# Kernel optimization log

Measured on AMD Instinct MI355X. Metric: run time of the kernel, lower is better.

Reference implementation:

```python
import jax, jax.numpy as jnp
import numpy as np

ODE_UNFOLDS = 6  # ncps LTCCell default
EPS = 1e-8


def setup_inputs() -> dict:
    key = jax.random.key(0)
    ks = jax.random.split(key, 24)
    B, C, H, W = 8192, 3, 23, 30   # 8*(H-1)*(W-1) = 5104 matches fc1
    S, N, M = 32, 19, 1            # sensory size, NCP units, motor outputs
    u = lambda k, shape, lo, hi: jax.random.uniform(k, shape, jnp.float32, lo, hi)
    # NCP wiring: binary sparsity masks (|adjacency|) and +/-1 reversal polarities
    sensory_mask = (jax.random.uniform(ks[20], (S, N)) < 0.6).astype(jnp.float32)
    mask = (jax.random.uniform(ks[21], (N, N)) < 0.5).astype(jnp.float32)
    sensory_erev = sensory_mask * jnp.sign(jax.random.normal(ks[22], (S, N)))
    erev = mask * jnp.sign(jax.random.normal(ks[23], (N, N)))
    return {
        "x": jax.random.normal(ks[0], (B, C, H, W), jnp.float32),
        "conv_w": jax.random.normal(ks[1], (8, C, 2, 2), jnp.float32) * 0.1,
        "conv_b": jnp.zeros((8,), jnp.float32),
        "fc1_w": jax.random.normal(ks[2], (64, 5104), jnp.float32) * 0.02,
        "fc1_b": jnp.zeros((64,), jnp.float32),
        "fc2_w": jax.random.normal(ks[3], (32, 64), jnp.float32) * 0.1,
        "fc2_b": jnp.zeros((32,), jnp.float32),
        "input_w": jnp.ones((S,), jnp.float32),
        "input_b": jnp.zeros((S,), jnp.float32),
        "sensory_w": u(ks[4], (S, N), 0.001, 1.0),
        "sensory_mu": u(ks[5], (S, N), 0.3, 0.8),
        "sensory_sigma": u(ks[6], (S, N), 3.0, 8.0),
        "sensory_erev": sensory_erev,
        "sensory_mask": sensory_mask,
        "w": u(ks[7], (N, N), 0.001, 1.0),
        "mu": u(ks[8], (N, N), 0.3, 0.8),
        "sigma": u(ks[9], (N, N), 3.0, 8.0),
        "erev": erev,
        "mask": mask,
        "gleak": u(ks[10], (N,), 0.001, 1.0),
        "vleak": u(ks[11], (N,), -0.2, 0.2),
        "cm": u(ks[12], (N,), 0.4, 0.6),
        "output_w": jnp.ones((M,), jnp.float32),
        "output_b": jnp.zeros((M,), jnp.float32),
    }


def _forward(x, conv_w, conv_b, fc1_w, fc1_b, fc2_w, fc2_b,
             input_w, input_b,
             sensory_w, sensory_mu, sensory_sigma, sensory_erev, sensory_mask,
             w, mu, sigma, erev, mask,
             gleak, vleak, cm, output_w, output_b):
    # conv + ELU
    y = jax.lax.conv_general_dilated(
        x, conv_w, window_strides=(1, 1), padding="VALID",
        dimension_numbers=("NCHW", "OIHW", "NCHW"))
    y = jax.nn.elu(y + conv_b[None, :, None, None])
    y = y.reshape(y.shape[0], -1)                 # (B, 5104)
    y = jax.nn.relu(y @ fc1_w.T + fc1_b)          # (B, 64); dropout = identity (eval)
    y = y @ fc2_w.T + fc2_b                       # (B, 32)

    # LTC: 2D input -> unbatched sequence of length B (ncps semantics)
    seq = y * input_w + input_b                   # affine input mapping, (T, S)
    # sensory synapse effects depend only on inputs -> precompute vectorized
    s_act = (jax.nn.softplus(sensory_w)
             * jax.nn.sigmoid(sensory_sigma * (seq[:, :, None] - sensory_mu))
             * sensory_mask)                      # (T, S, N)
    wnum_s = jnp.sum(s_act * sensory_erev, axis=1)  # (T, N)
    wden_s = jnp.sum(s_act, axis=1)                 # (T, N)

    cm_t = jax.nn.softplus(cm) * ODE_UNFOLDS      # cm / (elapsed_time=1 / unfolds)
    w_param = jax.nn.softplus(w) * mask           # (N, N), mask folded in
    g = jax.nn.softplus(gleak)

    def step(v, ins):
        wn_s, wd_s = ins
        for _ in range(ODE_UNFOLDS):              # implicit-Euler fused unfolds
            gate = jax.nn.sigmoid(sigma * (v[:, None] - mu))  # (src N, tgt N)
            w_act = w_param * gate
            wn = jnp.sum(w_act * erev, axis=0) + wn_s
            wd = jnp.sum(w_act, axis=0) + wd_s
            v = (cm_t * v + g * vleak + wn) / (cm_t + g + wd + EPS)
        return v, v

    v0 = jnp.zeros((w.shape[0],), seq.dtype)
    _, states = jax.lax.scan(step, v0, (wnum_s, wden_s))  # (T, N)
    # motor readout: first motor_size neurons + affine output mapping
    out = states[:, :output_w.shape[0]] * output_w + output_b  # (T, 1)
    return out


def reference(x, conv_w, conv_b, fc1_w, fc1_b, fc2_w, fc2_b,
              input_w, input_b,
              sensory_w, sensory_mu, sensory_sigma, sensory_erev, sensory_mask,
              w, mu, sigma, erev, mask,
              gleak, vleak, cm, output_w, output_b):
    return _forward(x, conv_w, conv_b, fc1_w, fc1_b, fc2_w, fc2_b,
                    input_w, input_b,
                    sensory_w, sensory_mu, sensory_sigma, sensory_erev, sensory_mask,
                    w, mu, sigma, erev, mask,
                    gleak, vleak, cm, output_w, output_b)
```

## Files before the change

kernel.cpp:

```cpp
#include <hip/hip_runtime.h>
#include <hip/hip_bf16.h>
#include <math.h>

#define L2E 1.4426950408889634f
#define T_STEPS 8192
#define KTOT 5104
#define EPS_LTC 1e-8f
#define KP 5120

#define SCAN_CHUNKS 1024
#define S_PER  8
#define WARM   16

#define WS_BASE_FLOATS 315584
#define WS_NEED_BSP    2573056

typedef __attribute__((ext_vector_type(8))) short bfrag;
typedef __attribute__((ext_vector_type(4))) float ffrag;
typedef __attribute__((ext_vector_type(4))) float fvec4;

__device__ __forceinline__ float softplus_f(float x) {
    return log1pf(expf(-fabsf(x))) + fmaxf(x, 0.f);
}

__device__ __forceinline__ unsigned short bf_hi(float f) {
    unsigned u = __float_as_uint(f);
    u = u + 0x7FFFu + ((u >> 16) & 1u);
    return (unsigned short)(u >> 16);
}

__device__ __forceinline__ float elu_f(float x) {
    return (x > 0.f) ? x : (__builtin_amdgcn_exp2f(x * L2E) - 1.f);
}

__device__ __forceinline__ float half_sum(float x) {
#if __has_builtin(__builtin_amdgcn_permlane32_swap)
    auto r = __builtin_amdgcn_permlane32_swap(__float_as_int(x), __float_as_int(x),
                                              false, false);
    return __int_as_float(r[0]) + __int_as_float(r[1]);
#else
    int pidx = ((threadIdx.x & 63) ^ 32) * 4;
    return x + __int_as_float(
        __builtin_amdgcn_ds_bpermute(pidx, __float_as_int(x)));
#endif
}

__global__ __launch_bounds__(640) void k0_combined(
    const float* __restrict__ sw, const float* __restrict__ smu,
    const float* __restrict__ ssig, const float* __restrict__ serev,
    const float* __restrict__ smask,
    const float* __restrict__ w, const float* __restrict__ mu,
    const float* __restrict__ sigma, const float* __restrict__ erev,
    const float* __restrict__ mask,
    const float* __restrict__ gleak, const float* __restrict__ vleak,
    const float* __restrict__ cm,
    float* __restrict__ sc1, float* __restrict__ sc0,
    float* __restrict__ swe, float* __restrict__ swp,
    float* __restrict__ rc1, float* __restrict__ rc0,
    float* __restrict__ rwe, float* __restrict__ rwp,
    float* __restrict__ neu,
    const float* __restrict__ fc1_w,
    unsigned short* __restrict__ bhi, unsigned short* __restrict__ blo,
    int use_bsp)
{
    if (blockIdx.x == 512) {
        int t = threadIdx.x;
        if (t < 608) {
            float sp = softplus_f(sw[t]);
            float c1 = ssig[t] * L2E;
            sc1[t] = c1;
            sc0[t] = c1 * smu[t];
            swe[t] = sp * serev[t];
            swp[t] = sp * smask[t];
        }
        if (t < 361) {
            float wp = softplus_f(w[t]) * mask[t];
            float c1 = sigma[t] * L2E;
            rc1[t] = c1;
            rc0[t] = c1 * mu[t];
            rwe[t] = wp * erev[t];
            rwp[t] = wp;
        }
        if (t < 64) {
            if (t < 19) {
                float g   = softplus_f(gleak[t]);
                float cmt = softplus_f(cm[t]) * 6.f;
                neu[t]       = cmt;
                neu[64 + t]  = g * vleak[t];
                neu[128 + t] = cmt + g + EPS_LTC;
            } else {
                neu[t] = 0.f; neu[64 + t] = 0.f; neu[128 + t] = 1.f;
            }
        }
        return;
    }
    if (!use_bsp) return;
    int i = blockIdx.x * 640 + threadIdx.x;
    int n, o, r;
    float v;
    if (i < 326656) {
        n = i / 5104;
        int k = i - n * 5104;
        o = k / 638;
        r = k - o * 638;
        v = fc1_w[i];
    } else {
        int p = i - 326656;
        n = p >> 4;
        int rem = p & 15;
        o = rem >> 1;
        r = 638 + (rem & 1);
        v = 0.f;
    }
    int kc = r >> 2, q = o >> 1;
    int j  = (o & 1) * 4 + (r & 3);
    int g  = (((kc * 16 + q * 4 + (n >> 4)) * 16) + (n & 15)) * 8 + j;
    unsigned short h = bf_hi(v);
    bhi[g] = h;
    blo[g] = bf_hi(v - __uint_as_float((unsigned)h << 16));
}

#define LOADWIN(KC, WB) do {                                                  \
    int r0_  = (KC) * 4;                                                      \
    int oh0_ = (r0_ * 565) >> 14;                                             \
    int ow0_ = r0_ - oh0_ * 29;                                               \
    _Pragma("unroll")                                                         \
    for (int cc_ = 0; cc_ < 3; cc_++) {                                       \
        const float* a0_ = xls + cc_ * 690 + oh0_ * 30 + ow0_;                \
        fvec4 v0_, v1_;                                                       \
        __builtin_memcpy(&v0_, a0_, 16);                                      \
        __builtin_memcpy(&v1_, a0_ + 30, 16);                                 \
        WB[cc_*10+0]=v0_.x; WB[cc_*10+1]=v0_.y; WB[cc_*10+2]=v0_.z;           \
        WB[cc_*10+3]=v0_.w; WB[cc_*10+4]=a0_[4];                              \
        WB[cc_*10+5]=v1_.x; WB[cc_*10+6]=v1_.y; WB[cc_*10+7]=v1_.z;           \
        WB[cc_*10+8]=v1_.w; WB[cc_*10+9]=a0_[34];                             \
    }                                                                         \
} while (0)

#define PACKA(Y0, Y1, AH, AL) do {                                            \
    _Pragma("unroll")                                                         \
    for (int j_ = 0; j_ < 4; j_++) {                                          \
        unsigned short h0_ = bf_hi(Y0[j_]);                                   \
        AH[j_] = (short)h0_;                                                  \
        AL[j_] = (short)bf_hi(Y0[j_] - __uint_as_float((unsigned)h0_ << 16)); \
        unsigned short h1_ = bf_hi(Y1[j_]);                                   \
        AH[4+j_] = (short)h1_;                                                \
        AL[4+j_] = (short)bf_hi(Y1[j_] - __uint_as_float((unsigned)h1_ << 16));\
    }                                                                         \
} while (0)

#define BUILDA_FAST(WB, AH, AL) do {                                          \
    float y0_[4], y1_[4];                                                     \
    _Pragma("unroll")                                                         \
    for (int rr_ = 0; rr_ < 4; rr_++) {                                       \
        float a0v_ = cb0, a1v_ = cb1;                                         \
        _Pragma("unroll")                                                     \
        for (int cc_ = 0; cc_ < 3; cc_++) {                                   \
            float x00_ = WB[cc_*10+rr_],   x01_ = WB[cc_*10+rr_+1];           \
            float x10_ = WB[cc_*10+5+rr_], x11_ = WB[cc_*10+6+rr_];           \
            a0v_ = fmaf(x00_, cw0[cc_*4+0], a0v_);                            \
            a0v_ = fmaf(x01_, cw0[cc_*4+1], a0v_);                            \
            a0v_ = fmaf(x10_, cw0[cc_*4+2], a0v_);                            \
            a0v_ = fmaf(x11_, cw0[cc_*4+3], a0v_);                            \
            a1v_ = fmaf(x00_, cw1[cc_*4+0], a1v_);                            \
            a1v_ = fmaf(x01_, cw1[cc_*4+1], a1v_);                            \
            a1v_ = fmaf(x10_, cw1[cc_*4+2], a1v_);                            \
            a1v_ = fmaf(x11_, cw1[cc_*4+3], a1v_);                            \
        }                                                                     \
        y0_[rr_] = elu_f(a0v_);                                               \
        y1_[rr_] = elu_f(a1v_);                                               \
    }                                                                         \
    PACKA(y0_, y1_, AH, AL);                                                  \
} while (0)

#define BUILDA_SLOW(KC, AH, AL) do {                                          \
    float y0_[4], y1_[4];                                                     \
    int r0_ = (KC) * 4;                                                       \
    _Pragma("unroll")                                                         \
    for (int rr_ = 0; rr_ < 4; rr_++) {                                       \
        int r_ = r0_ + rr_;                                                   \
        if (r_ < 638) {                                                       \
            int oh_ = (r_ * 565) >> 14;                                       \
            const float* xp_ = xls + oh_ * 30 + (r_ - oh_ * 29);              \
            float a0v_ = cb0, a1v_ = cb1;                                     \
            _Pragma("unroll")                                                 \
            for (int cc_ = 0; cc_ < 3; cc_++) {                               \
                float x00_ = xp_[cc_*690],    x01_ = xp_[cc_*690+1];          \
                float x10_ = xp_[cc_*690+30], x11_ = xp_[cc_*690+31];         \
                a0v_ = fmaf(x00_, cw0[cc_*4+0], a0v_);                        \
                a0v_ = fmaf(x01_, cw0[cc_*4+1], a0v_);                        \
                a0v_ = fmaf(x10_, cw0[cc_*4+2], a0v_);                        \
                a0v_ = fmaf(x11_, cw0[cc_*4+3], a0v_);                        \
                a1v_ = fmaf(x00_, cw1[cc_*4+0], a1v_);                        \
                a1v_ = fmaf(x01_, cw1[cc_*4+1], a1v_);                        \
                a1v_ = fmaf(x10_, cw1[cc_*4+2], a1v_);                        \
                a1v_ = fmaf(x11_, cw1[cc_*4+3], a1v_);                        \
            }                                                                 \
            y0_[rr_] = elu_f(a0v_);                                           \
            y1_[rr_] = elu_f(a1v_);                                           \
        } else { y0_[rr_] = 0.f; y1_[rr_] = 0.f; }                            \
    }                                                                         \
    PACKA(y0_, y1_, AH, AL);                                                  \
} while (0)

#define LOADB(KC, BH, BL) do {                                                \
    _Pragma("unroll")                                                         \
    for (int nt_ = 0; nt_ < 4; nt_++) {                                       \
        size_t off_ = ((size_t)((KC) * 16 + q * 4 + nt_) * 16 + mn) * 8;      \
        BH[nt_] = *(const bfrag*)(bhi + off_);                                \
        BL[nt_] = *(const bfrag*)(blo + off_);                                \
    }                                                                         \
} while (0)

#define MFMA3(AH, AL, BH, BL) do {                                            \
    _Pragma("unroll")                                                         \
    for (int nt_ = 0; nt_ < 4; nt_++) {                                       \
        acc[nt_] = __builtin_amdgcn_mfma_f32_16x16x32_bf16(AH, BH[nt_], acc[nt_], 0, 0, 0); \
        acc[nt_] = __builtin_amdgcn_mfma_f32_16x16x32_bf16(AH, BL[nt_], acc[nt_], 0, 0, 0); \
        acc[nt_] = __builtin_amdgcn_mfma_f32_16x16x32_bf16(AL, BH[nt_], acc[nt_], 0, 0, 0); \
    }                                                                         \
} while (0)

__global__ __launch_bounds__(512, 1) void k12_frontend(
    const float* __restrict__ x, const float* __restrict__ conv_w,
    const float* __restrict__ conv_b,
    const float* __restrict__ fc1_w, const float* __restrict__ fc1_b,
    const float* __restrict__ fc2_w, const float* __restrict__ fc2_b,
    const float* __restrict__ iw, const float* __restrict__ ib,
    const float* __restrict__ sc1, const float* __restrict__ sc0,
    const float* __restrict__ swe, const float* __restrict__ swp,
    const unsigned short* __restrict__ bhi,
    const unsigned short* __restrict__ blo, int use_bsp,
    float* __restrict__ wn_s, float* __restrict__ wd_s)
{
    __shared__ __align__(16) float smem[33120];
    float* redS = smem;
    float* hS   = smem + 8192;
    float* w2S  = smem + 9312;
    float* seqS = smem + 11392;

    const int t    = threadIdx.x;
    const int b0   = blockIdx.x * 16;
    const int lane = t & 63;
    const int wv   = t >> 6;
    const int q    = lane >> 4;
    const int mn   = lane & 15;
    const int o0   = 2 * q;

    {
        const float* xg = x + (size_t)b0 * 2070;
        #pragma unroll
        for (int i = 0; i < 16; i++) {
            int idx = i * 512 + t;
            fvec4 v;
            __builtin_memcpy(&v, xg + (size_t)idx * 4, 16);
            __builtin_memcpy(smem + (size_t)idx * 4, &v, 16);
        }
        if (t < 88) {
            int idx = 8192 + t;
            fvec4 v;
            __builtin_memcpy(&v, xg + (size_t)idx * 4, 16);
            __builtin_memcpy(smem + (size_t)idx * 4, &v, 16);
        }
    }
    __syncthreads();

    float cw0[12], cw1[12];
    #pragma unroll
    for (int i = 0; i < 12; i++) {
        cw0[i] = conv_w[o0 * 12 + i];
        cw1[i] = conv_w[o0 * 12 + 12 + i];
    }
    const float cb0 = conv_b[o0], cb1 = conv_b[o0 + 1];
    const float* xls = smem + mn * 2070;

    ffrag acc[4];
    #pragma unroll
    for (int nt = 0; nt < 4; nt++) acc[nt] = (ffrag){0.f, 0.f, 0.f, 0.f};

    const int kc0 = wv * 20;

    auto isFast = [](int kc) {
        int r0 = kc * 4;
        int oh0 = (r0 * 565) >> 14;
        int ow0 = r0 - oh0 * 29;
        return (ow0 <= 25 && r0 + 3 <= 637);
    };

    if (use_bsp) {
        float winA[30], winB[30];
        bfrag bh0[4], bl0[4], bh1[4], bl1[4];
        bool fA = isFast(kc0);
        if (fA) LOADWIN(kc0, winA);
        LOADB(kc0, bh0, bl0);
        for (int kk = 0; kk < 20; kk += 2) {
            const int kc = kc0 + kk;
            bool fB = isFast(kc + 1);
            LOADB(kc + 1, bh1, bl1);
            if (fB) LOADWIN(kc + 1, winB);
            {
                bfrag a_hi, a_lo;
                if (fA) { BUILDA_FAST(winA, a_hi, a_lo); }
                else    { BUILDA_SLOW(kc, a_hi, a_lo); }
                MFMA3(a_hi, a_lo, bh0, bl0);
            }
            fA = isFast(kc + 2);
            if (kk + 2 < 20) {
                LOADB(kc + 2, bh0, bl0);
                if (fA) LOADWIN(kc + 2, winA);
            }
            {
                bfrag a_hi, a_lo;
                if (fB) { BUILDA_FAST(winB, a_hi, a_lo); }
                else    { BUILDA_SLOW(kc + 1, a_hi, a_lo); }
                MFMA3(a_hi, a_lo, bh1, bl1);
            }
        }
    } else {
        for (int kk = 0; kk < 20; kk++) {
            const int kc = kc0 + kk;
            bfrag a_hi, a_lo;
            BUILDA_SLOW(kc, a_hi, a_lo);
            #pragma unroll
            for (int nt = 0; nt < 4; nt++) {
                int n = nt * 16 + mn;
                bfrag b_h, b_l;
                #pragma unroll
                for (int j = 0; j < 8; j++) {
                    int o = o0 + (j >> 2);
                    int r = kc * 4 + (j & 3);
                    float vv = (r < 638) ? fc1_w[(size_t)n * KTOT + o * 638 + r] : 0.f;
                    unsigned short h = bf_hi(vv);
                    b_h[j] = (short)h;
                    b_l[j] = (short)bf_hi(vv - __uint_as_float((unsigned)h << 16));
                }
                acc[nt] = __builtin_amdgcn_mfma_f32_16x16x32_bf16(a_hi, b_h, acc[nt], 0, 0, 0);
                acc[nt] = __builtin_amdgcn_mfma_f32_16x16x32_bf16(a_hi, b_l, acc[nt], 0, 0, 0);
                acc[nt] = __builtin_amdgcn_mfma_f32_16x16x32_bf16(a_lo, b_h, acc[nt], 0, 0, 0);
            }
        }
    }

    __syncthreads();

    #pragma unroll
    for (int nt = 0; nt < 4; nt++) {
        int n = nt * 16 + mn;
        #pragma unroll
        for (int rg = 0; rg < 4; rg++) {
            int m = q * 4 + rg;
            redS[(wv * 16 + m) * 64 + n] = acc[nt][rg];
        }
    }
    __syncthreads();
    #pragma unroll
    for (int e = 0; e < 2; e++) {
        int flat = e * 512 + t;
        int m = flat >> 6, n = flat & 63;
        float s = 0.f;
        #pragma unroll
        for (int p = 0; p < 8; p++) s += redS[(p * 16 + m) * 64 + n];
        hS[m * 68 + n] = fmaxf(s + fc1_b[n], 0.f);
    }
    #pragma unroll
    for (int e = 0; e < 4; e++) {
        int flat = e * 512 + t;
        int s = flat >> 6, n = flat & 63;
        w2S[s * 65 + n] = fc2_w[flat];
    }
    __syncthreads();

    {
        int s = t & 31, bl = t >> 5;
        float a2 = fc2_b[s];
        #pragma unroll 8
        for (int n = 0; n < 64; n++)
            a2 = fmaf(hS[bl * 68 + n], w2S[s * 65 + n], a2);
        seqS[bl * 33 + s] = a2 * iw[s] + ib[s];
    }
    __syncthreads();

    if (t < 304) {
        int n = t % 19, bl = t / 19;
        float wn = 0.f, wd = 0.f;
        #pragma unroll
        for (int s = 0; s < 32; s++) {
            float xx = sc0[s * 19 + n] - sc1[s * 19 + n] * seqS[bl * 33 + s];
            float ee = __builtin_amdgcn_exp2f(xx);
            float uu = __builtin_amdgcn_rcpf(1.f + ee);
            wn = fmaf(swe[s * 19 + n], uu, wn);
            wd = fmaf(swp[s * 19 + n], uu, wd);
        }
        wn_s[(b0 + bl) * 19 + n] = wn;
        wd_s[(b0 + bl) * 19 + n] = wd;
    }
}

__global__ __launch_bounds__(64, 1) void k3p2_scan(
    const float* __restrict__ wn_s, const float* __restrict__ wd_s,
    const float* __restrict__ rc1, const float* __restrict__ rc0,
    const float* __restrict__ rwe, const float* __restrict__ rwp,
    const float* __restrict__ neu,
    const float* __restrict__ out_w, const float* __restrict__ out_b,
    float* __restrict__ out)
{
    const int l    = threadIdx.x;
    const int col  = l & 31;
    const int p    = l >> 5;
    const int cidx = (col < 19) ? col : 0;
    const bool hi  = (l >= 32);

    float ca[10], cb[10], cwe[10], cwp[10];
    #pragma unroll
    for (int j = 0; j < 10; j++) {
        int s = p * 10 + j;
        bool e = (col < 19) && (s < 19);
        int idx = e ? (s * 19 + col) : 0;
        ca[j]  = e ? rc1[idx] : 0.f;
        cb[j]  = e ? rc0[idx] : 0.f;
        cwe[j] = e ? rwe[idx] : 0.f;
        cwp[j] = e ? rwp[idx] : 0.f;
    }

    const float cmt  = neu[cidx];
    const float gvl  = neu[64 + cidx];
    const float den0 = neu[128 + cidx];
    const float owv  = out_w[0];
    const float obv  = out_b[0];

    const int c       = blockIdx.x;
    const int s_out   = c * S_PER;
    const int s_begin = (s_out > WARM) ? (s_out - WARM) : 0;
    const int s_end   = s_out + S_PER;

    float v = 0.f;
    float wnc = wn_s[s_begin * 19 + cidx];
    float wdc = wd_s[s_begin * 19 + cidx];

    for (int tt = s_begin; tt < s_end; tt++) {
        int nt = (tt + 1 < T_STEPS) ? (tt + 1) : (T_STEPS - 1);
        float wnn = wn_s[nt * 19 + cidx];
        float wdn = wd_s[nt * 19 + cidx];

        #pragma unroll
        for (int u = 0; u < 6; u++) {
            float vs[10];
            #pragma unroll
            for (int j = 0; j < 10; j++) {
                float v0 = __int_as_float(
                    __builtin_amdgcn_readlane(__float_as_int(v), j));
                float v1 = __int_as_float(
                    __builtin_amdgcn_readlane(__float_as_int(v), 10 + j));
                vs[j] = hi ? v1 : v0;
            }

            float tn[10], td[10];
            #pragma unroll
            for (int j = 0; j < 10; j++) {
                float xx = fmaf(-ca[j], vs[j], cb[j]);
                float ee = __builtin_amdgcn_exp2f(xx);
                float uu = __builtin_amdgcn_rcpf(1.f + ee);
                tn[j] = cwe[j] * uu;
                td[j] = cwp[j] * uu;
            }
            float pn = (((tn[0] + tn[1]) + (tn[2] + tn[3]))
                      + ((tn[4] + tn[5]) + (tn[6] + tn[7])))
                      + (tn[8] + tn[9]);
            float pd = (((td[0] + td[1]) + (td[2] + td[3]))
                      + ((td[4] + td[5]) + (td[6] + td[7])))
                      + (td[8] + td[9]);

            pn = half_sum(pn);
            pd = half_sum(pd);

            float num = fmaf(cmt, v, gvl) + (pn + wnc);
            float den = den0 + pd + wdc;
            v = num * __builtin_amdgcn_rcpf(den);
        }
        if (l == 0 && tt >= s_out) out[tt] = fmaf(v, owv, obv);
        wnc = wnn; wdc = wdn;
    }
}

extern "C" void kernel_launch(void* const* d_in, const int* in_sizes, int n_in,
                              void* d_out, int out_size, void* d_ws, size_t ws_size,
                              hipStream_t stream) {
    const float* x      = (const float*)d_in[0];
    const float* conv_w = (const float*)d_in[1];
    const float* conv_b = (const float*)d_in[2];
    const float* fc1_w  = (const float*)d_in[3];
    const float* fc1_b  = (const float*)d_in[4];
    const float* fc2_w  = (const float*)d_in[5];
    const float* fc2_b  = (const float*)d_in[6];
    const float* iw     = (const float*)d_in[7];
    const float* ib     = (const float*)d_in[8];
    const float* sw     = (const float*)d_in[9];
    const float* smu    = (const float*)d_in[10];
    const float* ssig   = (const float*)d_in[11];
    const float* serev  = (const float*)d_in[12];
    const float* smask  = (const float*)d_in[13];
    const float* w      = (const float*)d_in[14];
    const float* mu     = (const float*)d_in[15];
    const float* sigma  = (const float*)d_in[16];
    const float* erev   = (const float*)d_in[17];
    const float* mask   = (const float*)d_in[18];
    const float* gleak  = (const float*)d_in[19];
    const float* vleak  = (const float*)d_in[20];
    const float* cm     = (const float*)d_in[21];
    const float* ow     = (const float*)d_in[22];
    const float* ob     = (const float*)d_in[23];

    float* ws   = (float*)d_ws;
    float* wn_s = ws;
    float* wd_s = wn_s + 155648;
    float* sc1  = wd_s + 155648;
    float* sc0  = sc1 + 640;
    float* swe  = sc0 + 640;
    float* swp  = swe + 640;
    float* rc1  = swp + 640;
    float* rc0  = rc1 + 384;
    float* rwe  = rc0 + 384;
    float* rwp  = rwe + 384;
    float* neu  = rwp + 384;
    const int use_bsp = (ws_size >= (size_t)WS_NEED_BSP) ? 1 : 0;
    unsigned short* bhi = (unsigned short*)(ws + WS_BASE_FLOATS);
    unsigned short* blo = bhi + 64 * KP;
    (void)in_sizes; (void)n_in; (void)out_size;

    hipLaunchKernelGGL(k0_combined, dim3(513), dim3(640), 0, stream,
        sw, smu, ssig, serev, smask, w, mu, sigma, erev, mask,
        gleak, vleak, cm, sc1, sc0, swe, swp, rc1, rc0, rwe, rwp, neu,
        fc1_w, bhi, blo, use_bsp);

    hipLaunchKernelGGL(k12_frontend, dim3(512), dim3(512), 0, stream,
        x, conv_w, conv_b, fc1_w, fc1_b, fc2_w, fc2_b, iw, ib,
        sc1, sc0, swe, swp, bhi, blo, use_bsp, wn_s, wd_s);

    hipLaunchKernelGGL(k3p2_scan, dim3(SCAN_CHUNKS), dim3(64), 0, stream,
        wn_s, wd_s, rc1, rc0, rwe, rwp, neu, ow, ob, (float*)d_out);
}
```

Before: 268.3 us.

## Read conv input directly from global, interleave K chunks, use bpermute in scan

The frontend kernel no longer stages the 16-sample input block into shared memory. Conv windows are read straight from global memory, which removes a barrier and shrinks LDS use from about 130KB to about 48KB. The K-chunk assignment changes from contiguous per-wave ranges to a stride-8 interleave across waves, and the barrier before the reduction writes is dropped. In the scan kernel, the 20 readlane calls plus select per unfold are replaced by 10 ds_bpermute gathers, trading scalar reads for LDS-crossbar traffic.

```diff
diff --git a/kernel.cpp b/kernel.cpp
--- a/kernel.cpp
+++ b/kernel.cpp
@@ -233,7 +233,7 @@
     const unsigned short* __restrict__ blo, int use_bsp,
     float* __restrict__ wn_s, float* __restrict__ wd_s)
 {
-    __shared__ __align__(16) float smem[33120];
+    __shared__ __align__(16) float smem[11920];
     float* redS = smem;
     float* hS   = smem + 8192;
     float* w2S  = smem + 9312;
@@ -247,24 +247,6 @@
     const int mn   = lane & 15;
     const int o0   = 2 * q;
 
-    {
-        const float* xg = x + (size_t)b0 * 2070;
-        #pragma unroll
-        for (int i = 0; i < 16; i++) {
-            int idx = i * 512 + t;
-            fvec4 v;
-            __builtin_memcpy(&v, xg + (size_t)idx * 4, 16);
-            __builtin_memcpy(smem + (size_t)idx * 4, &v, 16);
-        }
-        if (t < 88) {
-            int idx = 8192 + t;
-            fvec4 v;
-            __builtin_memcpy(&v, xg + (size_t)idx * 4, 16);
-            __builtin_memcpy(smem + (size_t)idx * 4, &v, 16);
-        }
-    }
-    __syncthreads();
-
     float cw0[12], cw1[12];
     #pragma unroll
     for (int i = 0; i < 12; i++) {
@@ -272,13 +254,11 @@
         cw1[i] = conv_w[o0 * 12 + 12 + i];
     }
     const float cb0 = conv_b[o0], cb1 = conv_b[o0 + 1];
-    const float* xls = smem + mn * 2070;
+    const float* xls = x + (size_t)(b0 + mn) * 2070;
 
     ffrag acc[4];
     #pragma unroll
     for (int nt = 0; nt < 4; nt++) acc[nt] = (ffrag){0.f, 0.f, 0.f, 0.f};
-
-    const int kc0 = wv * 20;
 
     auto isFast = [](int kc) {
         int r0 = kc * 4;
@@ -290,35 +270,36 @@
     if (use_bsp) {
         float winA[30], winB[30];
         bfrag bh0[4], bl0[4], bh1[4], bl1[4];
-        bool fA = isFast(kc0);
-        if (fA) LOADWIN(kc0, winA);
-        LOADB(kc0, bh0, bl0);
-        for (int kk = 0; kk < 20; kk += 2) {
-            const int kc = kc0 + kk;
-            bool fB = isFast(kc + 1);
-            LOADB(kc + 1, bh1, bl1);
-            if (fB) LOADWIN(kc + 1, winB);
+        bool fA = isFast(wv);
+        if (fA) LOADWIN(wv, winA);
+        LOADB(wv, bh0, bl0);
+        for (int i = 0; i < 20; i += 2) {
+            const int kcA = wv + 8 * i;
+            const int kcB = kcA + 8;
+            bool fB = isFast(kcB);
+            LOADB(kcB, bh1, bl1);
+            if (fB) LOADWIN(kcB, winB);
             {
                 bfrag a_hi, a_lo;
                 if (fA) { BUILDA_FAST(winA, a_hi, a_lo); }
-                else    { BUILDA_SLOW(kc, a_hi, a_lo); }
+                else    { BUILDA_SLOW(kcA, a_hi, a_lo); }
                 MFMA3(a_hi, a_lo, bh0, bl0);
             }
-            fA = isFast(kc + 2);
-            if (kk + 2 < 20) {
-                LOADB(kc + 2, bh0, bl0);
-                if (fA) LOADWIN(kc + 2, winA);
+            fA = (i + 2 < 20) && isFast(kcA + 16);
+            if (i + 2 < 20) {
+                LOADB(kcA + 16, bh0, bl0);
+                if (fA) LOADWIN(kcA + 16, winA);
             }
             {
                 bfrag a_hi, a_lo;
                 if (fB) { BUILDA_FAST(winB, a_hi, a_lo); }
-                else    { BUILDA_SLOW(kc + 1, a_hi, a_lo); }
+                else    { BUILDA_SLOW(kcB, a_hi, a_lo); }
                 MFMA3(a_hi, a_lo, bh1, bl1);
             }
         }
     } else {
-        for (int kk = 0; kk < 20; kk++) {
-            const int kc = kc0 + kk;
+        for (int i = 0; i < 20; i++) {
+            const int kc = wv + 8 * i;
             bfrag a_hi, a_lo;
             BUILDA_SLOW(kc, a_hi, a_lo);
             #pragma unroll
@@ -341,8 +322,6 @@
         }
     }
 
-    __syncthreads();
-
     #pragma unroll
     for (int nt = 0; nt < 4; nt++) {
         int n = nt * 16 + mn;
@@ -408,9 +387,9 @@
     const int col  = l & 31;
     const int p    = l >> 5;
     const int cidx = (col < 19) ? col : 0;
-    const bool hi  = (l >= 32);
 
     float ca[10], cb[10], cwe[10], cwp[10];
+    int gidx[10];
     #pragma unroll
     for (int j = 0; j < 10; j++) {
         int s = p * 10 + j;
@@ -420,6 +399,7 @@
         cb[j]  = e ? rc0[idx] : 0.f;
         cwe[j] = e ? rwe[idx] : 0.f;
         cwp[j] = e ? rwp[idx] : 0.f;
+        gidx[j] = ((s < 19) ? s : 0) * 4;
     }
 
     const float cmt  = neu[cidx];
@@ -446,13 +426,9 @@
         for (int u = 0; u < 6; u++) {
             float vs[10];
             #pragma unroll
-            for (int j = 0; j < 10; j++) {
-                float v0 = __int_as_float(
-                    __builtin_amdgcn_readlane(__float_as_int(v), j));
-                float v1 = __int_as_float(
-                    __builtin_amdgcn_readlane(__float_as_int(v), 10 + j));
-                vs[j] = hi ? v1 : v0;
-            }
+            for (int j = 0; j < 10; j++)
+                vs[j] = __int_as_float(
+                    __builtin_amdgcn_ds_bpermute(gidx[j], __float_as_int(v)));
 
             float tn[10], td[10];
             #pragma unroll
```

Result: slower. 322.5 us (+20.2%).
